# Kernel tuning notes

Measured on AMD Instinct MI355X. Metric: run time of the kernel, lower is better.

Reference implementation:

```python
import jax, jax.numpy as jnp
import numpy as np

TEMPERATURE = 0.07
NEG_RATIO = 1.0
ADJ_DENSITY = 0.002
SAMPLE_SEED = 42


def setup_inputs() -> dict:
    key = jax.random.key(0)
    k1, k2, k3 = jax.random.split(key, 3)
    I, E, D = 4096, 16384, 64
    item = jax.random.normal(k1, (I, D), dtype=jnp.float32)
    ent = jax.random.normal(k2, (E, D), dtype=jnp.float32)
    # sparse binary adjacency: ~33 positives per item on average
    adj = (jax.random.uniform(k3, (I, E)) < ADJ_DENSITY).astype(jnp.int32)
    return {"item_embeddings": item, "entity_embeddings": ent, "adj_matrix": adj}


def reference(item_embeddings, entity_embeddings, adj_matrix):
    # L2-normalize rows, cosine similarity / temperature
    it = item_embeddings / jnp.linalg.norm(item_embeddings, axis=1, keepdims=True)
    en = entity_embeddings / jnp.linalg.norm(entity_embeddings, axis=1, keepdims=True)
    sim = jnp.einsum('id,ed->ie', it, en) / TEMPERATURE  # [I, E]

    pos_mask = adj_matrix > 0                             # [I, E]
    neg_mask = ~pos_mask
    num_pos = pos_mask.sum(axis=1)                        # [I]
    num_neg = neg_mask.sum(axis=1)
    # num_negatives = min(int(num_pos * ratio), num_neg)  (per item)
    k = jnp.minimum(jnp.floor(num_pos.astype(jnp.float32) * NEG_RATIO).astype(jnp.int32), num_neg)

    # negative sampling without replacement: uniform keys, take k smallest among negatives
    u = jax.random.uniform(jax.random.key(SAMPLE_SEED), sim.shape)
    u = jnp.where(pos_mask, jnp.inf, u)                   # positives rank last
    rank = jnp.argsort(jnp.argsort(u, axis=1), axis=1)    # per-row rank of each entity
    samp = (rank < k[:, None]) & neg_mask                 # sampled negatives [I, E]

    valid = (num_pos > 0) & (k > 0)                       # items contributing pairs

    # stable per-item logsumexp over sampled negatives
    neg_logits = jnp.where(samp, sim, -jnp.inf)
    m = jnp.max(neg_logits, axis=1)                       # [I], -inf if no sampled negs
    m_safe = jnp.where(valid, m, 0.0)
    S = jnp.sum(jnp.where(samp, jnp.exp(sim - m_safe[:, None]), 0.0), axis=1)  # [I]

    # per positive pair: CE with pos as class 0 over [pos, sampled_negs]
    # loss = log(exp(pos) + sum exp(neg)) - pos, stabilized with pairwise max
    pm = jnp.maximum(sim, m_safe[:, None])
    loss_pair = jnp.log(jnp.exp(sim - pm) + S[:, None] * jnp.exp(m_safe[:, None] - pm)) + pm - sim

    pair_mask = pos_mask & valid[:, None]
    total = jnp.sum(jnp.where(pair_mask, loss_pair, 0.0))
    n_pairs = jnp.sum(jnp.where(valid, num_pos, 0))
    return jnp.where(n_pairs > 0, total / jnp.maximum(n_pairs, 1).astype(jnp.float32), 0.0)
```

## Files before the change

kernel.cpp:

```cpp
#include <hip/hip_runtime.h>
#include <math.h>


constexpr int D      = 64;
constexpr int PCAP   = 96;
constexpr int CCAP   = 192;
constexpr int SELCAP = 128;

typedef int int4v __attribute__((ext_vector_type(4)));

__device__ __forceinline__ void threefry2x32(unsigned x0, unsigned x1,
                                             unsigned& o0, unsigned& o1) {
  const unsigned ks0 = 0u;
  const unsigned ks1 = 42u;
  const unsigned ks2 = 0x1BD11BDAu ^ 0u ^ 42u;
  x0 += ks0; x1 += ks1;
#define TF_R(r) { x0 += x1; x1 = (x1 << (r)) | (x1 >> (32 - (r))); x1 ^= x0; }
  TF_R(13) TF_R(15) TF_R(26) TF_R(6)
  x0 += ks1; x1 += ks2 + 1u;
  TF_R(17) TF_R(29) TF_R(16) TF_R(24)
  x0 += ks2; x1 += ks0 + 2u;
  TF_R(13) TF_R(15) TF_R(26) TF_R(6)
  x0 += ks0; x1 += ks1 + 3u;
  TF_R(17) TF_R(29) TF_R(16) TF_R(24)
  x0 += ks1; x1 += ks2 + 4u;
  TF_R(13) TF_R(15) TF_R(26) TF_R(6)
  x0 += ks2; x1 += ks0 + 5u;
#undef TF_R
  o0 = x0; o1 = x1;
}

__device__ __forceinline__ int lane_prior(unsigned long long m) {
  return (int)__builtin_amdgcn_mbcnt_hi(
      (unsigned)(m >> 32), __builtin_amdgcn_mbcnt_lo((unsigned)m, 0u));
}

__device__ __forceinline__ void wave_append(bool pred, int e,
                                            int* cnt, int* list, int cap) {
  unsigned long long m = __ballot(pred);
  if (m) {
    const int lane = threadIdx.x & 63;
    const int leader = __builtin_ctzll(m);
    int base = 0;
    if (lane == leader) base = atomicAdd(cnt, (int)__popcll(m));
    base = __builtin_amdgcn_readlane(base, leader);
    if (pred) {
      int s = base + lane_prior(m);
      if (s < cap) list[s] = e;
    }
  }
}

__device__ __forceinline__ void wave_append2(bool pred, int e, unsigned key,
                                             int* cnt, int* li, unsigned* lk,
                                             int cap) {
  unsigned long long m = __ballot(pred);
  if (m) {
    const int lane = threadIdx.x & 63;
    const int leader = __builtin_ctzll(m);
    int base = 0;
    if (lane == leader) base = atomicAdd(cnt, (int)__popcll(m));
    base = __builtin_amdgcn_readlane(base, leader);
    if (pred) {
      int s = base + lane_prior(m);
      if (s < cap) { li[s] = e; lk[s] = key; }
    }
  }
}

__device__ __forceinline__ float dot_sim(const float* __restrict__ ent, int e,
                                         const float* itemn) {
  const float4* er = (const float4*)(ent + ((size_t)e << 6));
  float dot = 0.f, ss = 0.f;
#pragma unroll
  for (int q = 0; q < 16; ++q) {
    float4 f = er[q];
    dot += itemn[4 * q + 0] * f.x + itemn[4 * q + 1] * f.y +
           itemn[4 * q + 2] * f.z + itemn[4 * q + 3] * f.w;
    ss += f.x * f.x + f.y * f.y + f.z * f.z + f.w * f.w;
  }
  return dot * (1.0f / sqrtf(ss));
}

__device__ __forceinline__ float block_max(float v, float* wred, int t) {
#pragma unroll
  for (int off = 32; off; off >>= 1) v = fmaxf(v, __shfl_xor(v, off, 64));
  __syncthreads();
  if ((t & 63) == 0) wred[t >> 6] = v;
  __syncthreads();
  return fmaxf(fmaxf(wred[0], wred[1]), fmaxf(wred[2], wred[3]));
}

__device__ __forceinline__ float block_sum(float v, float* wred, int t) {
#pragma unroll
  for (int off = 32; off; off >>= 1) v += __shfl_xor(v, off, 64);
  __syncthreads();
  if ((t & 63) == 0) wred[t >> 6] = v;
  __syncthreads();
  return wred[0] + wred[1] + wred[2] + wred[3];
}

template <bool WSOUT>
__global__ __launch_bounds__(256) void infonce_mono(
    const float* __restrict__ item, const float* __restrict__ ent,
    const int* __restrict__ adj, int I, int E,
    float* __restrict__ loss, int* __restrict__ cnt,
    double* __restrict__ accum, int* __restrict__ paircnt) {
  const int t = threadIdx.x;
  const int halfI = I >> 1;
  const int iA = blockIdx.x;
  const int iB = iA + halfI;
  const unsigned HALF = (unsigned)halfI * (unsigned)E;
  const unsigned baseA = (unsigned)iA * (unsigned)E;

  __shared__ int s_pos[2][PCAP];
  __shared__ int s_ci[2][CCAP];
  __shared__ unsigned s_ck[2][CCAP];
  __shared__ int s_sel[SELCAP];
  __shared__ int s_hist[256];
  __shared__ float s_itemn[D];
  __shared__ float s_wred[4];
  __shared__ int s_np[2], s_nc[2];
  __shared__ int s_nsel, s_bbin, s_cbef, s_fnc;
  __shared__ float s_scale;

  if (t < 2) { s_np[t] = 0; s_nc[t] = 0; }
  __syncthreads();

  const int nvec = E >> 2;
  const int4v* adjA = (const int4v*)(adj + (size_t)iA * E);
  const int4v* adjB = (const int4v*)(adj + (size_t)iB * E);
  int4v a4 = __builtin_nontemporal_load(&adjA[t]);
  int4v b4 = __builtin_nontemporal_load(&adjB[t]);
  for (int v = t; v < nvec; v += 256) {
    int4v an, bn;
    const int vn = v + 256;
    if (vn < nvec) {
      an = __builtin_nontemporal_load(&adjA[vn]);
      bn = __builtin_nontemporal_load(&adjB[vn]);
    }
    const unsigned e0 = (unsigned)v * 4u;
    unsigned o0[4], o1[4];
#pragma unroll
    for (int c = 0; c < 4; ++c) {
      const unsigned x = baseA + e0 + c;
      threefry2x32(x, x + HALF, o0[c], o1[c]);
    }
#pragma unroll
    for (int c = 0; c < 4; ++c) {
      const int e = (int)(e0 + c);
      const bool pa = (a4[c] > 0), pb = (b4[c] > 0);
      wave_append(pa, e, &s_np[0], s_pos[0], PCAP);
      wave_append(pb, e, &s_np[1], s_pos[1], PCAP);
      wave_append2(!pa && o0[c] < (1u << 24), e, o0[c] >> 9,
                   &s_nc[0], s_ci[0], s_ck[0], CCAP);
      wave_append2(!pb && o1[c] < (1u << 24), e, o1[c] >> 9,
                   &s_nc[1], s_ci[1], s_ck[1], CCAP);
    }
    a4 = an; b4 = bn;
  }
  __syncthreads();

  for (int r2 = 0; r2 < 2; ++r2) {
    const int row = r2 ? iB : iA;
    const int npos = min(s_np[r2], PCAP);
    const int k = min(npos, E - npos);
    const bool valid = (npos > 0 && k > 0);
    float rowloss = 0.f;
    if (valid) {
      if (t == 0) s_nsel = 0;
      __syncthreads();
      int ncand = min(s_nc[r2], CCAP);
      int rneed = k;
      if (s_nc[r2] > CCAP || ncand < k) {
        s_hist[t] = 0;
        if (t == 0) s_fnc = 0;
        __syncthreads();
        const int* adjR = adj + (size_t)row * E;
        for (int e = t; e < E; e += 256) {
          if (adjR[e] > 0) continue;
          unsigned o0, o1;
          threefry2x32(baseA + (unsigned)e, baseA + (unsigned)e + HALF, o0, o1);
          atomicAdd(&s_hist[(r2 ? o1 : o0) >> 24], 1);
        }
        __syncthreads();
        if (t == 0) {
          int cum = 0, b = 0;
          while (b < 255 && cum + s_hist[b] < k) { cum += s_hist[b]; ++b; }
          s_bbin = b; s_cbef = cum;
        }
        __syncthreads();
        const int b = s_bbin;
        for (int e = t; e < E; e += 256) {
          bool neg = (adjR[e] <= 0);
          unsigned o0, o1, bits = 0xFFFFFFFFu;
          if (neg) {
            threefry2x32(baseA + (unsigned)e, baseA + (unsigned)e + HALF, o0, o1);
            bits = r2 ? o1 : o0;
          }
          int b8 = (int)(bits >> 24);
          wave_append(neg && b8 < b, e, &s_nsel, s_sel, SELCAP);
          wave_append2(neg && b8 == b, e, bits >> 9,
                       &s_fnc, s_ci[r2], s_ck[r2], CCAP);
        }
        __syncthreads();
        ncand = min(s_fnc, CCAP);
        rneed = k - s_cbef;
      }

      for (int i = t; i < ncand; i += 256) {
        const unsigned mk = s_ck[r2][i];
        const int mi = s_ci[r2][i];
        int rank = 0;
        for (int c = 0; c < ncand; ++c) {
          const unsigned ck = s_ck[r2][c];
          const int ci = s_ci[r2][c];
          rank += (ck < mk || (ck == mk && ci < mi)) ? 1 : 0;
        }
        if (rank < rneed) {
          int s = atomicAdd(&s_nsel, 1);
          if (s < SELCAP) s_sel[s] = mi;
        }
      }

      float iv = 0.f;
      if (t < D) iv = item[(size_t)row * D + t];
      if (t < 64) {
        float ss = iv * iv;
#pragma unroll
        for (int off = 32; off; off >>= 1) ss += __shfl_xor(ss, off, 64);
        if (t == 0) s_scale = (1.0f / sqrtf(ss)) * (1.0f / 0.07f);
      }
      __syncthreads();
      if (t < D) s_itemn[t] = iv * s_scale;
      __syncthreads();
      const int nsel = min(s_nsel, SELCAP);

      float myv = (t < nsel) ? dot_sim(ent, s_sel[t], s_itemn) : -INFINITY;
      const float m = block_max(myv, s_wred, t);
      float v2 = (t < nsel) ? expf(myv - m) : 0.f;
      const float S = block_sum(v2, s_wred, t);

      float lp = 0.f;
      if (t < npos) {
        float sp = dot_sim(ent, s_pos[r2][t], s_itemn);
        float pm = fmaxf(sp, m);
        lp = logf(expf(sp - pm) + S * expf(m - pm)) + pm - sp;
      }
      rowloss = block_sum(lp, s_wred, t);
    }
    if (WSOUT) {
      if (t == 0) { loss[row] = valid ? rowloss : 0.f; cnt[row] = valid ? npos : 0; }
    } else {
      if (valid && t == 0) {
        atomicAdd(accum, (double)rowloss);
        atomicAdd(paircnt, npos);
      }
    }
    __syncthreads();
  }
}

__global__ __launch_bounds__(256) void reduce_out(
    const float* __restrict__ loss, const int* __restrict__ cnt, int I,
    float* __restrict__ out) {
  const int t = threadIdx.x;
  __shared__ double s_l[256];
  __shared__ int s_n[256];
  double l = 0.0;
  int n = 0;
  for (int i = t; i < I; i += 256) { l += (double)loss[i]; n += cnt[i]; }
  s_l[t] = l; s_n[t] = n;
  __syncthreads();
  for (int off = 128; off; off >>= 1) {
    if (t < off) { s_l[t] += s_l[t + off]; s_n[t] += s_n[t + off]; }
    __syncthreads();
  }
  if (t == 0) out[0] = (s_n[0] > 0) ? (float)(s_l[0] / (double)s_n[0]) : 0.f;
}

__global__ void infonce_init(double* accum, int* cnt) {
  if (threadIdx.x == 0 && blockIdx.x == 0) { accum[0] = 0.0; cnt[0] = 0; }
}

__global__ void infonce_final(const double* __restrict__ accum,
                              const int* __restrict__ cnt,
                              float* __restrict__ out) {
  if (threadIdx.x == 0 && blockIdx.x == 0) {
    int n = cnt[0];
    out[0] = (n > 0) ? (float)(accum[0] / (double)n) : 0.f;
  }
}

extern "C" void kernel_launch(void* const* d_in, const int* in_sizes, int n_in,
                              void* d_out, int out_size, void* d_ws, size_t ws_size,
                              hipStream_t stream) {
  const float* item = (const float*)d_in[0];
  const float* ent  = (const float*)d_in[1];
  const int*   adj  = (const int*)d_in[2];
  const int I = in_sizes[0] / D;
  const int E = in_sizes[1] / D;

  const size_t need = (size_t)I * 8;
  if (ws_size >= need && (I % 2) == 0) {
    float* loss = (float*)d_ws;
    int*   cnt  = (int*)(loss + I);
    infonce_mono<true><<<I / 2, 256, 0, stream>>>(item, ent, adj, I, E,
                                                  loss, cnt, nullptr, nullptr);
    reduce_out<<<1, 256, 0, stream>>>(loss, cnt, I, (float*)d_out);
  } else {
    double* accum   = (double*)d_ws;
    int*    paircnt = (int*)((char*)d_ws + 8);
    infonce_init<<<1, 64, 0, stream>>>(accum, paircnt);
    infonce_mono<false><<<I / 2, 256, 0, stream>>>(item, ent, adj, I, E,
                                                   nullptr, nullptr, accum, paircnt);
    infonce_final<<<1, 64, 0, stream>>>(accum, paircnt, (float*)d_out);
  }
}
```

Measured before the change: 158.4 us.

## Pack positive flags into per-thread bitmasks and hoist item normalization

During the adjacency scan, positives are no longer appended per element through wave ballots. Each thread now packs them into a 64-bit bitmask and flushes them once at the end with a single atomic per thread. Item normalization for both rows is done once up front by two waves, removing per-row syncs, and the rotate uses a builtin. A fallback path rescans adjacency when the positive count overflows the cap, so correctness holds beyond PCAP. The trade-off is that positive ordering is no longer sequential and the fast path requires E divisible by 1024 and at most 16384.

Measured after the change: 173.8 us. 9.8% more time.

```diff
diff --git a/kernel.cpp b/kernel.cpp
--- a/kernel.cpp
+++ b/kernel.cpp
@@ -8,6 +8,7 @@
 constexpr int SELCAP = 128;
 
 typedef int int4v __attribute__((ext_vector_type(4)));
+typedef unsigned long long u64;
 
 __device__ __forceinline__ void threefry2x32(unsigned x0, unsigned x1,
                                              unsigned& o0, unsigned& o1) {
@@ -15,7 +16,7 @@
   const unsigned ks1 = 42u;
   const unsigned ks2 = 0x1BD11BDAu ^ 0u ^ 42u;
   x0 += ks0; x1 += ks1;
-#define TF_R(r) { x0 += x1; x1 = (x1 << (r)) | (x1 >> (32 - (r))); x1 ^= x0; }
+#define TF_R(r) { x0 += x1; x1 = __builtin_rotateleft32(x1, (r)) ^ x0; }
   TF_R(13) TF_R(15) TF_R(26) TF_R(6)
   x0 += ks1; x1 += ks2 + 1u;
   TF_R(17) TF_R(29) TF_R(16) TF_R(24)
@@ -118,27 +119,30 @@
   __shared__ unsigned s_ck[2][CCAP];
   __shared__ int s_sel[SELCAP];
   __shared__ int s_hist[256];
-  __shared__ float s_itemn[D];
+  __shared__ float s_itemn[2][D];
   __shared__ float s_wred[4];
   __shared__ int s_np[2], s_nc[2];
   __shared__ int s_nsel, s_bbin, s_cbef, s_fnc;
-  __shared__ float s_scale;
 
   if (t < 2) { s_np[t] = 0; s_nc[t] = 0; }
-  __syncthreads();
-
-  const int nvec = E >> 2;
+  if (t < 128) {
+    const int r = t >> 6, ln = t & 63;
+    float iv = item[(size_t)(r ? iB : iA) * D + ln];
+    float ss = iv * iv;
+#pragma unroll
+    for (int off = 32; off; off >>= 1) ss += __shfl_xor(ss, off, 64);
+    s_itemn[r][ln] = iv * (1.0f / sqrtf(ss)) * (1.0f / 0.07f);
+  }
+  __syncthreads();
+
+  const int niter = E >> 10;
+  u64 wposA = 0, wposB = 0;
   const int4v* adjA = (const int4v*)(adj + (size_t)iA * E);
   const int4v* adjB = (const int4v*)(adj + (size_t)iB * E);
-  int4v a4 = __builtin_nontemporal_load(&adjA[t]);
-  int4v b4 = __builtin_nontemporal_load(&adjB[t]);
-  for (int v = t; v < nvec; v += 256) {
-    int4v an, bn;
-    const int vn = v + 256;
-    if (vn < nvec) {
-      an = __builtin_nontemporal_load(&adjA[vn]);
-      bn = __builtin_nontemporal_load(&adjB[vn]);
-    }
+  for (int i = 0; i < niter; ++i) {
+    const int v = t + (i << 8);
+    int4v a4 = __builtin_nontemporal_load(&adjA[v]);
+    int4v b4 = __builtin_nontemporal_load(&adjB[v]);
     const unsigned e0 = (unsigned)v * 4u;
     unsigned o0[4], o1[4];
 #pragma unroll
@@ -146,33 +150,62 @@
       const unsigned x = baseA + e0 + c;
       threefry2x32(x, x + HALF, o0[c], o1[c]);
     }
+    const unsigned nibA = (a4[0] & 1) | ((a4[1] & 1) << 1) |
+                          ((a4[2] & 1) << 2) | ((a4[3] & 1) << 3);
+    const unsigned nibB = (b4[0] & 1) | ((b4[1] & 1) << 1) |
+                          ((b4[2] & 1) << 2) | ((b4[3] & 1) << 3);
+    wposA |= (u64)nibA << (4 * i);
+    wposB |= (u64)nibB << (4 * i);
 #pragma unroll
     for (int c = 0; c < 4; ++c) {
       const int e = (int)(e0 + c);
-      const bool pa = (a4[c] > 0), pb = (b4[c] > 0);
-      wave_append(pa, e, &s_np[0], s_pos[0], PCAP);
-      wave_append(pb, e, &s_np[1], s_pos[1], PCAP);
-      wave_append2(!pa && o0[c] < (1u << 24), e, o0[c] >> 9,
+      wave_append2(!((nibA >> c) & 1) && (o0[c] >> 24) == 0u, e, o0[c] >> 9,
                    &s_nc[0], s_ci[0], s_ck[0], CCAP);
-      wave_append2(!pb && o1[c] < (1u << 24), e, o1[c] >> 9,
+      wave_append2(!((nibB >> c) & 1) && (o1[c] >> 24) == 0u, e, o1[c] >> 9,
                    &s_nc[1], s_ci[1], s_ck[1], CCAP);
     }
-    a4 = an; b4 = bn;
+  }
+  {
+    const int nA = (int)__popcll(wposA);
+    if (nA) {
+      int base = atomicAdd(&s_np[0], nA);
+      u64 w = wposA;
+      for (int j = 0; w; ++j) {
+        const int b = (int)__builtin_ctzll(w);
+        w &= w - 1;
+        const int e = ((b >> 2) << 10) + (t << 2) + (b & 3);
+        if (base + j < PCAP) s_pos[0][base + j] = e;
+      }
+    }
+    const int nB = (int)__popcll(wposB);
+    if (nB) {
+      int base = atomicAdd(&s_np[1], nB);
+      u64 w = wposB;
+      for (int j = 0; w; ++j) {
+        const int b = (int)__builtin_ctzll(w);
+        w &= w - 1;
+        const int e = ((b >> 2) << 10) + (t << 2) + (b & 3);
+        if (base + j < PCAP) s_pos[1][base + j] = e;
+      }
+    }
   }
   __syncthreads();
 
   for (int r2 = 0; r2 < 2; ++r2) {
     const int row = r2 ? iB : iA;
-    const int npos = min(s_np[r2], PCAP);
-    const int k = min(npos, E - npos);
-    const bool valid = (npos > 0 && k > 0);
+    const int npT = s_np[r2];
+    const int npos = min(npT, PCAP);
+    const int k = min(npT, E - npT);
+    const bool valid = (npT > 0 && k > 0);
     float rowloss = 0.f;
+    bool fb = false;
     if (valid) {
       if (t == 0) s_nsel = 0;
       __syncthreads();
       int ncand = min(s_nc[r2], CCAP);
       int rneed = k;
-      if (s_nc[r2] > CCAP || ncand < k) {
+      fb = (s_nc[r2] > CCAP) || (ncand < k) || (npT > PCAP);
+      if (fb) {
         s_hist[t] = 0;
         if (t == 0) s_fnc = 0;
         __syncthreads();
@@ -222,39 +255,39 @@
           if (s < SELCAP) s_sel[s] = mi;
         }
       }
-
-      float iv = 0.f;
-      if (t < D) iv = item[(size_t)row * D + t];
-      if (t < 64) {
-        float ss = iv * iv;
-#pragma unroll
-        for (int off = 32; off; off >>= 1) ss += __shfl_xor(ss, off, 64);
-        if (t == 0) s_scale = (1.0f / sqrtf(ss)) * (1.0f / 0.07f);
-      }
-      __syncthreads();
-      if (t < D) s_itemn[t] = iv * s_scale;
       __syncthreads();
       const int nsel = min(s_nsel, SELCAP);
 
-      float myv = (t < nsel) ? dot_sim(ent, s_sel[t], s_itemn) : -INFINITY;
+      float myv = (t < nsel) ? dot_sim(ent, s_sel[t], s_itemn[r2]) : -INFINITY;
       const float m = block_max(myv, s_wred, t);
       float v2 = (t < nsel) ? expf(myv - m) : 0.f;
       const float S = block_sum(v2, s_wred, t);
 
       float lp = 0.f;
-      if (t < npos) {
-        float sp = dot_sim(ent, s_pos[r2][t], s_itemn);
-        float pm = fmaxf(sp, m);
-        lp = logf(expf(sp - pm) + S * expf(m - pm)) + pm - sp;
+      if (!fb) {
+        if (t < npos) {
+          float sp = dot_sim(ent, s_pos[r2][t], s_itemn[r2]);
+          float pm = fmaxf(sp, m);
+          lp = logf(expf(sp - pm) + S * expf(m - pm)) + pm - sp;
+        }
+      } else {
+        const int* adjR = adj + (size_t)row * E;
+        for (int e = t; e < E; e += 256) {
+          if (adjR[e] > 0) {
+            float sp = dot_sim(ent, e, s_itemn[r2]);
+            float pm = fmaxf(sp, m);
+            lp += logf(expf(sp - pm) + S * expf(m - pm)) + pm - sp;
+          }
+        }
       }
       rowloss = block_sum(lp, s_wred, t);
     }
     if (WSOUT) {
-      if (t == 0) { loss[row] = valid ? rowloss : 0.f; cnt[row] = valid ? npos : 0; }
+      if (t == 0) { loss[row] = valid ? rowloss : 0.f; cnt[row] = valid ? npT : 0; }
     } else {
       if (valid && t == 0) {
         atomicAdd(accum, (double)rowloss);
-        atomicAdd(paircnt, npos);
+        atomicAdd(paircnt, npT);
       }
     }
     __syncthreads();
@@ -302,12 +335,12 @@
   const int E = in_sizes[1] / D;
 
   const size_t need = (size_t)I * 8;
-  if (ws_size >= need && (I % 2) == 0) {
-    float* loss = (float*)d_ws;
-    int*   cnt  = (int*)(loss + I);
+  if (ws_size >= need && (I % 2) == 0 && (E % 1024) == 0 && E <= 16384) {
+    float* lossb = (float*)d_ws;
+    int*   cntb  = (int*)(lossb + I);
     infonce_mono<true><<<I / 2, 256, 0, stream>>>(item, ent, adj, I, E,
-                                                  loss, cnt, nullptr, nullptr);
-    reduce_out<<<1, 256, 0, stream>>>(loss, cnt, I, (float*)d_out);
+                                                  lossb, cntb, nullptr, nullptr);
+    reduce_out<<<1, 256, 0, stream>>>(lossb, cntb, I, (float*)d_out);
   } else {
     double* accum   = (double*)d_ws;
     int*    paircnt = (int*)((char*)d_ws + 8);
```
